# Optimization experiments

Hardware: AMD Instinct MI355X
Metric: run time of the kernel (lower is better)

## Reference

```python
import jax, jax.numpy as jnp
import numpy as np

H, W = 256, 336
FLOW_SCALING = float(max(H, W))  # max(config['loader']['resolution'])
REG_WEIGHT = 0.001               # config['loss']['flow_regul_weight']
B, N = 8, 262144


def setup_inputs() -> dict:
    key = jax.random.key(0)
    k1, k2, k3, k4, k5 = jax.random.split(key, 5)
    # small flow so a reasonable fraction of warped events stays in-bounds
    flow = 0.05 * jax.random.normal(k1, (B, 2, H, W), dtype=jnp.float32)
    ys = jax.random.randint(k2, (B, N), 0, H).astype(jnp.float32)
    xs = jax.random.randint(k3, (B, N), 0, W).astype(jnp.float32)
    ts = jax.random.uniform(k4, (B, N), dtype=jnp.float32)  # normalized timestamps in [0,1]
    pol = jax.random.randint(k5, (B, N), 0, 2)
    # event layout per the code: (ts, y, x, p)
    event_list = jnp.stack([ts, ys, xs, pol.astype(jnp.float32) * 2.0 - 1.0], axis=-1)
    pol_mask = jnp.stack([(pol == 1), (pol == 0)], axis=-1).astype(jnp.float32)  # [B,N,2]
    return {"flow": flow, "event_list": event_list, "pol_mask": pol_mask}


def _get_interpolation(events, event_flow, tref):
    # warped event coords (y, x): [B, N, 2]
    warped = events[:, :, 1:3] + (tref - events[:, :, 0:1]) * event_flow * FLOW_SCALING
    top_y = jnp.floor(warped[:, :, 0:1])
    bot_y = jnp.floor(warped[:, :, 0:1] + 1.0)
    left_x = jnp.floor(warped[:, :, 1:2])
    right_x = jnp.floor(warped[:, :, 1:2] + 1.0)
    # four bilinear corners stacked along event dim -> [B, 4N, 2]
    idx = jnp.concatenate([
        jnp.concatenate([top_y, left_x], -1),
        jnp.concatenate([top_y, right_x], -1),
        jnp.concatenate([bot_y, left_x], -1),
        jnp.concatenate([bot_y, right_x], -1)], axis=1)
    warped4 = jnp.tile(warped, (1, 4, 1))
    weights = jnp.maximum(0.0, 1.0 - jnp.abs(warped4 - idx))
    mask = ((idx[:, :, 0:1] >= 0) & (idx[:, :, 0:1] < H)
            & (idx[:, :, 1:2] >= 0) & (idx[:, :, 1:2] < W)).astype(weights.dtype)
    idx = idx * mask          # unfeasible indices -> 0
    weights = weights * mask  # unfeasible weights -> 0
    flat_idx = (idx[:, :, 0] * W + idx[:, :, 1]).astype(jnp.int32)  # [B, 4N]
    w = jnp.prod(weights, axis=-1, keepdims=True)                    # [B, 4N, 1]
    return flat_idx, w


def _interpolate(flat_idx, weights, polarity_mask):
    # scatter-add bilinear weights into an H*W image, per batch element
    w = (weights * polarity_mask)[:, :, 0]  # [B, 4N]
    return jax.vmap(lambda i, v: jax.ops.segment_sum(v, i, num_segments=H * W))(flat_idx, w)


def reference(flow, event_list, pol_mask):
    pol4 = jnp.tile(pol_mask, (1, 4, 1))              # [B, 4N, 2]
    ts4 = jnp.tile(event_list[:, :, 0:1], (1, 4, 1))  # [B, 4N, 1]
    # gather flow at original event pixel locations
    flow_idx = (event_list[:, :, 1] * W + event_list[:, :, 2]).astype(jnp.int32)  # [B, N]
    flow_flat = flow.reshape(flow.shape[0], 2, -1)
    event_flowy = jnp.take_along_axis(flow_flat[:, 1, :], flow_idx, axis=1)
    event_flowx = jnp.take_along_axis(flow_flat[:, 0, :], flow_idx, axis=1)
    event_flow = jnp.stack([event_flowy, event_flowx], axis=-1)  # [B, N, 2] (y, x)

    loss = jnp.float32(0.0)
    # forward warp (tref=1, avg ts) and backward warp (tref=0, avg 1-ts)
    for tref, tgrad in ((1.0, ts4), (0.0, 1.0 - ts4)):
        idx, wts = _get_interpolation(event_list, event_flow, tref)
        for p in range(2):  # positive / negative polarity
            pm = pol4[:, :, p:p + 1]
            iwe = _interpolate(idx, wts, pm)
            iwe_ts = _interpolate(idx, wts * tgrad, pm)
            loss = loss + jnp.sum((iwe_ts / (iwe + 1e-9)) ** 2)

    # charbonnier flow smoothness
    flow_dx = flow[:, :, :-1, :] - flow[:, :, 1:, :]
    flow_dy = flow[:, :, :, :-1] - flow[:, :, :, 1:]
    smooth = jnp.sum(jnp.sqrt(flow_dx ** 2 + 1e-6)) + jnp.sum(jnp.sqrt(flow_dy ** 2 + 1e-6))
    return loss + REG_WEIGHT * smooth
```

## Files before the change

### kernel.cpp

```cpp
#include <hip/hip_runtime.h>

#define HH 256
#define WW 336
#define HWPIX (HH * WW)
#define BATCH 8
#define NEV 262144
#define NEV_SHIFT 18
#define FLOW_SCALING 336.0f
#define REG_WEIGHT 0.001f

#define BANDS 32
#define BANDSHIFT 3
#define BANDROWS 8
#define NBINS (2 * BATCH * BANDS)
#define CAP 14336
#define GSTRIDE 16

#define BE_THREADS 1024
#define EVPT 2
#define EV_PER_BLOCK (BE_THREADS * EVPT)
#define MAXITEMS 8320

#define HTILE (BANDROWS * WW)
#define NBLK_ACC NBINS

#define GCOUNT_BYTES (NBINS * GSTRIDE * 4)
#define PK_BYTES ((size_t)NBINS * CAP * 4)
#define QY_BYTES ((size_t)NBINS * CAP * 2)

__device__ __forceinline__ float wave_reduce_sum(float v) {
    #pragma unroll
    for (int o = 32; o > 0; o >>= 1) v += __shfl_down(v, o, 64);
    return v;
}

__device__ __forceinline__ float charb(float d) { return sqrtf(d * d + 1e-6f); }

__global__ __launch_bounds__(256)
void flow_prep(const float* __restrict__ flow, float2* __restrict__ flowi,
               unsigned int* __restrict__ gcount, float* __restrict__ loss_acc,
               unsigned int* __restrict__ done_count,
               float* __restrict__ smooth_partial) {
    __shared__ float red[4];
    int tid = threadIdx.x;
    if (blockIdx.x == 0) {
        for (int i = tid; i < NBINS * GSTRIDE; i += 256) gcount[i] = 0u;
        if (tid == 0) { *loss_acc = 0.0f; *done_count = 0u; }
    }

    const int N4 = BATCH * HWPIX / 4;
    const int H4 = HWPIX / 4;
    const int W4 = WW / 4;
    float v = 0.0f;
    for (int i = blockIdx.x * 256 + tid; i < N4; i += gridDim.x * 256) {
        int b = i / H4, u = i - b * H4;
        int row = u / W4, c4 = u - row * W4;
        const float4* ch0 = (const float4*)(flow + (size_t)b * 2 * HWPIX);
        const float4* ch1 = ch0 + H4;
        float4 a0 = ch0[u];
        float4 a1 = ch1[u];

        float4* fo = (float4*)(flowi + (size_t)b * HWPIX);
        fo[2 * u]     = make_float4(a0.x, a1.x, a0.y, a1.y);
        fo[2 * u + 1] = make_float4(a0.z, a1.z, a0.w, a1.w);

        if (row < HH - 1) {
            float4 d0 = ch0[u + W4];
            float4 d1 = ch1[u + W4];
            v += charb(a0.x - d0.x) + charb(a0.y - d0.y) +
                 charb(a0.z - d0.z) + charb(a0.w - d0.w) +
                 charb(a1.x - d1.x) + charb(a1.y - d1.y) +
                 charb(a1.z - d1.z) + charb(a1.w - d1.w);
        }
        v += charb(a0.x - a0.y) + charb(a0.y - a0.z) + charb(a0.z - a0.w) +
             charb(a1.x - a1.y) + charb(a1.y - a1.z) + charb(a1.z - a1.w);
        if (c4 < W4 - 1) {
            float r0 = ((const float*)ch0)[4 * u + 4];
            float r1 = ((const float*)ch1)[4 * u + 4];
            v += charb(a0.w - r0) + charb(a1.w - r1);
        }
    }
    v = wave_reduce_sum(v);
    if ((tid & 63) == 0) red[tid >> 6] = v;
    __syncthreads();
    if (tid < 4) {
        float r = red[tid];
        r += __shfl_down(r, 2, 64);
        r += __shfl_down(r, 1, 64);
        if (tid == 0) smooth_partial[blockIdx.x] = r;
    }
}

__global__ __launch_bounds__(BE_THREADS)
void bin_events(const float2* __restrict__ flowi,
                const float4* __restrict__ ev,
                unsigned int* __restrict__ gcount,
                unsigned int* __restrict__ pk_arr,
                unsigned short* __restrict__ qy_arr) {
    __shared__ int lcnt[64];
    __shared__ int loff[64];
    __shared__ int gbase[64];
    __shared__ int stotal;
    __shared__ __align__(16) unsigned long long sval[MAXITEMS];

    int tid = threadIdx.x;
    if (tid < 64) lcnt[tid] = 0;
    __syncthreads();

    int base = blockIdx.x * EV_PER_BLOCK;
    int b = base >> NEV_SHIFT;
    const float2* fB = flowi + (size_t)b * HWPIX;

    unsigned int pkv[EVPT][2];
    unsigned int hiA[EVPT][2], hiB[EVPT][2];
    int rkA[EVPT][2], rkB[EVPT][2];

    #pragma unroll
    for (int e = 0; e < EVPT; ++e) {
        int bn = base + e * BE_THREADS + tid;
        float4 ee = ev[bn];
        float t = ee.x, y = ee.y, x = ee.z;
        unsigned int p = (ee.w > 0.0f) ? 0u : 1u;

        int iy = (int)y, ix = (int)x;
        float2 f = fB[iy * WW + ix];
        float fx = f.x, fy = f.y;

        #pragma unroll
        for (int tr = 0; tr < 2; ++tr) {
            rkA[e][tr] = -1; rkB[e][tr] = -1;
            float tref  = tr ? 0.0f : 1.0f;
            float tg    = tr ? (1.0f - t) : t;
            float dtS = (tref - t) * FLOW_SCALING;
            float wy = fmaf(dtS, fy, y);
            float wx = fmaf(dtS, fx, x);
            if (!(wx > -1.0f && wx < (float)WW)) continue;
            if (!(wy > -1.0f && wy < (float)HH)) continue;

            int ty = (int)floorf(wy);
            int band0 = -1, band1 = -1;
            if (ty >= 0 && ty < HH) band0 = ty >> BANDSHIFT;
            int r1 = ty + 1;
            if (r1 >= 0 && r1 < HH) {
                int bb = r1 >> BANDSHIFT;
                if (bb != band0) band1 = bb;
            }

            unsigned int qx = (unsigned int)(fmaf(wx, 2048.0f, 2048.5f));
            unsigned int qt = (unsigned int)(tg * 2047.0f + 0.5f);
            pkv[e][tr] = (qx << 12) | (qt << 1) | p;

            if (band0 >= 0) {
                float wyrel = wy - (float)(band0 * BANDROWS - 1);
                unsigned int qy = (unsigned int)fmaf(wyrel, 2048.0f, 0.5f);
                int lb = tr * BANDS + band0;
                hiA[e][tr] = qy | ((unsigned int)lb << 16);
                rkA[e][tr] = atomicAdd(&lcnt[lb], 1);
            }
            if (band1 >= 0) {
                float wyrel = wy - (float)(band1 * BANDROWS - 1);
                unsigned int qy = (unsigned int)fmaf(wyrel, 2048.0f, 0.5f);
                int lb = tr * BANDS + band1;
                hiB[e][tr] = qy | ((unsigned int)lb << 16);
                rkB[e][tr] = atomicAdd(&lcnt[lb], 1);
            }
        }
    }
    __syncthreads();

    if (tid < 64) {
        int c  = lcnt[tid];
        int ce = (c + 1) & ~1;
        int xg = ce;
        #pragma unroll
        for (int o = 1; o < 64; o <<= 1) {
            int yv = __shfl_up(xg, o, 64);
            if (tid >= o) xg += yv;
        }
        int lo = xg - ce;
        loff[tid] = lo;
        if (tid == 63) stotal = xg;
        int gbin = ((tid >> 5) * BATCH + b) * BANDS + (tid & 31);
        gbase[tid] = ce > 0 ? (int)atomicAdd(&gcount[gbin * GSTRIDE],
                                             (unsigned int)ce) : 0;
        if (c & 1) {
            unsigned int hi = (15u << 11) | ((unsigned int)tid << 16);
            sval[lo + c] = ((unsigned long long)hi << 32);
        }
    }
    __syncthreads();

    #pragma unroll
    for (int e = 0; e < EVPT; ++e) {
        #pragma unroll
        for (int tr = 0; tr < 2; ++tr) {
            if (rkA[e][tr] >= 0) {
                int lb = (hiA[e][tr] >> 16) & 63;
                sval[loff[lb] + rkA[e][tr]] =
                    (unsigned long long)pkv[e][tr] |
                    ((unsigned long long)hiA[e][tr] << 32);
            }
            if (rkB[e][tr] >= 0) {
                int lb = (hiB[e][tr] >> 16) & 63;
                sval[loff[lb] + rkB[e][tr]] =
                    (unsigned long long)pkv[e][tr] |
                    ((unsigned long long)hiB[e][tr] << 32);
            }
        }
    }
    __syncthreads();

    int total = stotal;
    for (int i = tid * 2; i < total; i += 2 * BE_THREADS) {
        uint4 two = *(const uint4*)&sval[i];
        unsigned int pk0 = two.x, h0 = two.y;
        unsigned int qy0 = h0 & 0xffffu;
        int lb0 = (h0 >> 16) & 63;
        int gs0 = gbase[lb0] + (i - loff[lb0]);
        int gbin0 = ((lb0 >> 5) * BATCH + b) * BANDS + (lb0 & 31);
        if (gs0 + 1 < CAP) {
            size_t s = (size_t)gbin0 * CAP + gs0;
            *(uint2*)(pk_arr + s) = make_uint2(pk0, two.z);
            *(unsigned int*)(qy_arr + s) = qy0 | ((two.w & 0xffffu) << 16);
        }
    }
}

__device__ __forceinline__ unsigned int pack_w(float w, float tg) {
    unsigned int lo16 = (unsigned int)fmaf(w, 1024.0f, 0.5f);
    unsigned int hi16 = (unsigned int)fmaf(w * tg, 1024.0f, 0.5f);
    return lo16 | (hi16 << 16);
}

__device__ __forceinline__ void accum_item(unsigned int* __restrict__ sA,
                                           unsigned int* __restrict__ sB,
                                           unsigned int pk, unsigned int qy) {
    unsigned int qx = pk >> 12;
    float tg = (float)((pk >> 1) & 2047u) * (1.0f / 2047.0f);
    int p = pk & 1u;

    int lx = (int)(qx >> 11) - 1;
    float fxx = (float)(qx & 2047u) * (1.0f / 2048.0f);

    int rowq = qy >> 11;
    float fy = (float)(qy & 2047u) * (1.0f / 2048.0f);
    int row_top = rowq - 1;

    unsigned int* A  = sA + p * HTILE;
    unsigned int* Bb = sB + p * HTILE;

    #pragma unroll
    for (int a = 0; a < 2; ++a) {
        int ry = row_top + a;
        if ((unsigned)ry >= (unsigned)BANDROWS) continue;
        float wrow = a ? fy : (1.0f - fy);
        int rb = ry * WW;
        if (lx >= 0 && lx + 1 < WW) {
            unsigned int pl = pack_w(wrow * (1.0f - fxx), tg);
            unsigned int pr = pack_w(wrow * fxx, tg);
            unsigned long long v =
                (unsigned long long)pl | ((unsigned long long)pr << 32);
            if (v == 0ull) continue;
            if ((lx & 1) == 0) {
                atomicAdd((unsigned long long*)(A + rb + lx), v);
            } else {
                atomicAdd((unsigned long long*)(Bb + rb + lx - 1), v);
            }
        } else if (lx == -1) {
            unsigned int pw = pack_w(wrow * fxx, tg);
            if (pw) atomicAdd(&A[rb], pw);
        } else if (lx == WW - 1) {
            unsigned int pw = pack_w(wrow * (1.0f - fxx), tg);
            if (pw) atomicAdd(&A[rb + lx], pw);
        }
    }
}

__global__ __launch_bounds__(1024)
void bin_accum(const unsigned int* __restrict__ gcount,
               const unsigned int* __restrict__ pk_arr,
               const unsigned short* __restrict__ qy_arr,
               const float* __restrict__ smooth_partial,
               float* __restrict__ loss_acc,
               unsigned int* __restrict__ done_count,
               float* __restrict__ out) {
    __shared__ __align__(16) unsigned int sA[2 * HTILE];
    __shared__ __align__(16) unsigned int sB[2 * HTILE];
    __shared__ float red[16];
    __shared__ int lastflag;

    int band = blockIdx.x;
    int tr   = blockIdx.y;
    int b    = blockIdx.z;
    int tid  = threadIdx.x;

    for (int i = tid; i < 2 * HTILE; i += 1024) { sA[i] = 0u; sB[i] = 0u; }
    __syncthreads();

    int gbin = (tr * BATCH + b) * BANDS + band;
    int cnt = min((int)gcount[gbin * GSTRIDE], CAP);
    const unsigned int* pkp = pk_arr + (size_t)gbin * CAP;
    const unsigned short* qyp = qy_arr + (size_t)gbin * CAP;
    const uint4* pk4 = (const uint4*)pkp;
    const uint4* qy8 = (const uint4*)qyp;

    int noct = cnt >> 3;
    if (tid < noct) {
        uint4 p0 = pk4[2 * tid], p1 = pk4[2 * tid + 1];
        uint4 q0 = qy8[tid];
        for (int n = tid + 1024; n < noct; n += 1024) {
            uint4 np0 = pk4[2 * n], np1 = pk4[2 * n + 1];
            uint4 nq0 = qy8[n];
            accum_item(sA, sB, p0.x, q0.x & 0xffffu);
            accum_item(sA, sB, p0.y, q0.x >> 16);
            accum_item(sA, sB, p0.z, q0.y & 0xffffu);
            accum_item(sA, sB, p0.w, q0.y >> 16);
            accum_item(sA, sB, p1.x, q0.z & 0xffffu);
            accum_item(sA, sB, p1.y, q0.z >> 16);
            accum_item(sA, sB, p1.z, q0.w & 0xffffu);
            accum_item(sA, sB, p1.w, q0.w >> 16);
            p0 = np0; p1 = np1; q0 = nq0;
        }
        accum_item(sA, sB, p0.x, q0.x & 0xffffu);
        accum_item(sA, sB, p0.y, q0.x >> 16);
        accum_item(sA, sB, p0.z, q0.y & 0xffffu);
        accum_item(sA, sB, p0.w, q0.y >> 16);
        accum_item(sA, sB, p1.x, q0.z & 0xffffu);
        accum_item(sA, sB, p1.y, q0.z >> 16);
        accum_item(sA, sB, p1.z, q0.w & 0xffffu);
        accum_item(sA, sB, p1.w, q0.w >> 16);
    }
    int done = noct << 3;
    int rem = cnt - done;
    if (tid < rem) {
        accum_item(sA, sB, pkp[done + tid], (unsigned int)qyp[done + tid]);
    }
    __syncthreads();

    float v = 0.0f;
    for (int i = tid; i < 2 * HTILE; i += 1024) {
        int px = i - (i / WW) * WW;
        unsigned int u = sA[i] + (px ? sB[i - 1] : 0u);
        float iwe = (float)(u & 0xffffu);
        float its = (float)(u >> 16);
        float r = its / (iwe + 1.024e-6f);
        v += r * r;
    }
    v = wave_reduce_sum(v);
    if ((tid & 63) == 0) red[tid >> 6] = v;
    __syncthreads();
    if (tid == 0) {
        float r = 0.0f;
        #pragma unroll
        for (int k = 0; k < 16; ++k) r += red[k];
        atomicAdd(loss_acc, r);
        __threadfence();
        unsigned int t = atomicAdd(done_count, 1u);
        lastflag = (t == (unsigned)(NBLK_ACC - 1));
    }
    __syncthreads();

    if (lastflag) {
        float pv = (tid < 512) ? smooth_partial[tid] : 0.0f;
        pv = wave_reduce_sum(pv);
        if ((tid & 63) == 0) red[tid >> 6] = pv;
        __syncthreads();
        if (tid == 0) {
            float sm = 0.0f;
            #pragma unroll
            for (int k = 0; k < 16; ++k) sm += red[k];
            float total = atomicAdd(loss_acc, 0.0f);
            *out = total + REG_WEIGHT * sm;
        }
    }
}

extern "C" void kernel_launch(void* const* d_in, const int* in_sizes, int n_in,
                              void* d_out, int out_size, void* d_ws, size_t ws_size,
                              hipStream_t stream) {
    const float*  flow  = (const float*)d_in[0];
    const float4* ev    = (const float4*)d_in[1];
    float* out = (float*)d_out;

    unsigned int*   gcount     = (unsigned int*)d_ws;
    float*          loss_acc   = (float*)((char*)d_ws + GCOUNT_BYTES);
    unsigned int*   done_count = (unsigned int*)((char*)d_ws + GCOUNT_BYTES + 4);
    float*          smooth_p   = (float*)((char*)d_ws + GCOUNT_BYTES + 512);
    unsigned int*   pk_arr     = (unsigned int*)((char*)d_ws + GCOUNT_BYTES + 4096);
    unsigned short* qy_arr     = (unsigned short*)((char*)d_ws + GCOUNT_BYTES + 4096 + PK_BYTES);
    float2*         flowi      = (float2*)((char*)d_ws + GCOUNT_BYTES + 4096 + PK_BYTES + QY_BYTES);

    flow_prep<<<512, 256, 0, stream>>>(flow, flowi, gcount, loss_acc,
                                       done_count, smooth_p);

    int total_ev = BATCH * NEV;
    bin_events<<<total_ev / EV_PER_BLOCK, BE_THREADS, 0, stream>>>(
        flowi, ev, gcount, pk_arr, qy_arr);

    dim3 g2(BANDS, 2, BATCH);
    bin_accum<<<g2, 1024, 0, stream>>>(gcount, pk_arr, qy_arr, smooth_p,
                                       loss_acc, done_count, out);
}
```

Before: 133.9 us.

## Move smoothness term into accumulation kernel and widen bin padding to four

The Charbonnier smoothness reduction moves out of flow_prep and into bin_accum, where each block handles a strided slice of the flow and folds the weighted sum into its loss contribution. This leaves flow_prep as a pure transpose and removes the separate partial-sum array and the final-block reduction. Bin counts are now padded to multiples of four instead of two, so the scatter from shared memory can write 16-byte pk and 8-byte qy stores, at the cost of more dummy padding items and a slightly larger shared buffer. The added flow reads in bin_accum may overlap with its atomic-heavy accumulation phase, but they also lengthen that kernel.

Result: no change. 133.3 us, median of 2 (-0.4%).

```diff
diff --git a/kernel.cpp b/kernel.cpp
--- a/kernel.cpp
+++ b/kernel.cpp
@@ -19,7 +19,7 @@
 #define BE_THREADS 1024
 #define EVPT 2
 #define EV_PER_BLOCK (BE_THREADS * EVPT)
-#define MAXITEMS 8320
+#define MAXITEMS 8384
 
 #define HTILE (BANDROWS * WW)
 #define NBLK_ACC NBINS
@@ -39,9 +39,7 @@
 __global__ __launch_bounds__(256)
 void flow_prep(const float* __restrict__ flow, float2* __restrict__ flowi,
                unsigned int* __restrict__ gcount, float* __restrict__ loss_acc,
-               unsigned int* __restrict__ done_count,
-               float* __restrict__ smooth_partial) {
-    __shared__ float red[4];
+               unsigned int* __restrict__ done_count) {
     int tid = threadIdx.x;
     if (blockIdx.x == 0) {
         for (int i = tid; i < NBINS * GSTRIDE; i += 256) gcount[i] = 0u;
@@ -50,11 +48,8 @@
 
     const int N4 = BATCH * HWPIX / 4;
     const int H4 = HWPIX / 4;
-    const int W4 = WW / 4;
-    float v = 0.0f;
     for (int i = blockIdx.x * 256 + tid; i < N4; i += gridDim.x * 256) {
         int b = i / H4, u = i - b * H4;
-        int row = u / W4, c4 = u - row * W4;
         const float4* ch0 = (const float4*)(flow + (size_t)b * 2 * HWPIX);
         const float4* ch1 = ch0 + H4;
         float4 a0 = ch0[u];
@@ -63,31 +58,6 @@
         float4* fo = (float4*)(flowi + (size_t)b * HWPIX);
         fo[2 * u]     = make_float4(a0.x, a1.x, a0.y, a1.y);
         fo[2 * u + 1] = make_float4(a0.z, a1.z, a0.w, a1.w);
-
-        if (row < HH - 1) {
-            float4 d0 = ch0[u + W4];
-            float4 d1 = ch1[u + W4];
-            v += charb(a0.x - d0.x) + charb(a0.y - d0.y) +
-                 charb(a0.z - d0.z) + charb(a0.w - d0.w) +
-                 charb(a1.x - d1.x) + charb(a1.y - d1.y) +
-                 charb(a1.z - d1.z) + charb(a1.w - d1.w);
-        }
-        v += charb(a0.x - a0.y) + charb(a0.y - a0.z) + charb(a0.z - a0.w) +
-             charb(a1.x - a1.y) + charb(a1.y - a1.z) + charb(a1.z - a1.w);
-        if (c4 < W4 - 1) {
-            float r0 = ((const float*)ch0)[4 * u + 4];
-            float r1 = ((const float*)ch1)[4 * u + 4];
-            v += charb(a0.w - r0) + charb(a1.w - r1);
-        }
-    }
-    v = wave_reduce_sum(v);
-    if ((tid & 63) == 0) red[tid >> 6] = v;
-    __syncthreads();
-    if (tid < 4) {
-        float r = red[tid];
-        r += __shfl_down(r, 2, 64);
-        r += __shfl_down(r, 1, 64);
-        if (tid == 0) smooth_partial[blockIdx.x] = r;
     }
 }
 
@@ -170,7 +140,7 @@
 
     if (tid < 64) {
         int c  = lcnt[tid];
-        int ce = (c + 1) & ~1;
+        int ce = (c + 3) & ~3;
         int xg = ce;
         #pragma unroll
         for (int o = 1; o < 64; o <<= 1) {
@@ -183,10 +153,9 @@
         int gbin = ((tid >> 5) * BATCH + b) * BANDS + (tid & 31);
         gbase[tid] = ce > 0 ? (int)atomicAdd(&gcount[gbin * GSTRIDE],
                                              (unsigned int)ce) : 0;
-        if (c & 1) {
-            unsigned int hi = (15u << 11) | ((unsigned int)tid << 16);
-            sval[lo + c] = ((unsigned long long)hi << 32);
-        }
+        unsigned int hi = (15u << 11) | ((unsigned int)tid << 16);
+        for (int j = c; j < ce; ++j)
+            sval[lo + j] = ((unsigned long long)hi << 32);
     }
     __syncthreads();
 
@@ -211,17 +180,18 @@
     __syncthreads();
 
     int total = stotal;
-    for (int i = tid * 2; i < total; i += 2 * BE_THREADS) {
-        uint4 two = *(const uint4*)&sval[i];
-        unsigned int pk0 = two.x, h0 = two.y;
-        unsigned int qy0 = h0 & 0xffffu;
-        int lb0 = (h0 >> 16) & 63;
+    for (int i = tid * 4; i < total; i += 4 * BE_THREADS) {
+        uint4 q0 = *(const uint4*)&sval[i];
+        uint4 q1 = *(const uint4*)&sval[i + 2];
+        int lb0 = (q0.y >> 16) & 63;
         int gs0 = gbase[lb0] + (i - loff[lb0]);
         int gbin0 = ((lb0 >> 5) * BATCH + b) * BANDS + (lb0 & 31);
-        if (gs0 + 1 < CAP) {
+        if (gs0 + 3 < CAP) {
             size_t s = (size_t)gbin0 * CAP + gs0;
-            *(uint2*)(pk_arr + s) = make_uint2(pk0, two.z);
-            *(unsigned int*)(qy_arr + s) = qy0 | ((two.w & 0xffffu) << 16);
+            *(uint4*)(pk_arr + s) = make_uint4(q0.x, q0.z, q1.x, q1.z);
+            *(uint2*)(qy_arr + s) = make_uint2(
+                (q0.y & 0xffffu) | ((q0.w & 0xffffu) << 16),
+                (q1.y & 0xffffu) | ((q1.w & 0xffffu) << 16));
         }
     }
 }
@@ -280,7 +250,7 @@
 void bin_accum(const unsigned int* __restrict__ gcount,
                const unsigned int* __restrict__ pk_arr,
                const unsigned short* __restrict__ qy_arr,
-               const float* __restrict__ smooth_partial,
+               const float* __restrict__ flow,
                float* __restrict__ loss_acc,
                unsigned int* __restrict__ done_count,
                float* __restrict__ out) {
@@ -293,6 +263,7 @@
     int tr   = blockIdx.y;
     int b    = blockIdx.z;
     int tid  = threadIdx.x;
+    int lblk = band + 32 * (tr + 2 * b);
 
     for (int i = tid; i < 2 * HTILE; i += 1024) { sA[i] = 0u; sB[i] = 0u; }
     __syncthreads();
@@ -335,6 +306,36 @@
     if (tid < rem) {
         accum_item(sA, sB, pkp[done + tid], (unsigned int)qyp[done + tid]);
     }
+
+    float sm = 0.0f;
+    {
+        const int N4 = BATCH * HWPIX / 4;
+        const int H4 = HWPIX / 4;
+        const int W4 = WW / 4;
+        for (int i = lblk * 1024 + tid; i < N4; i += NBLK_ACC * 1024) {
+            int bb = i / H4, u = i - bb * H4;
+            int row = u / W4, c4 = u - row * W4;
+            const float4* ch0 = (const float4*)(flow + (size_t)bb * 2 * HWPIX);
+            const float4* ch1 = ch0 + H4;
+            float4 a0 = ch0[u];
+            float4 a1 = ch1[u];
+            if (row < HH - 1) {
+                float4 d0 = ch0[u + W4];
+                float4 d1 = ch1[u + W4];
+                sm += charb(a0.x - d0.x) + charb(a0.y - d0.y) +
+                      charb(a0.z - d0.z) + charb(a0.w - d0.w) +
+                      charb(a1.x - d1.x) + charb(a1.y - d1.y) +
+                      charb(a1.z - d1.z) + charb(a1.w - d1.w);
+            }
+            sm += charb(a0.x - a0.y) + charb(a0.y - a0.z) + charb(a0.z - a0.w) +
+                  charb(a1.x - a1.y) + charb(a1.y - a1.z) + charb(a1.z - a1.w);
+            if (c4 < W4 - 1) {
+                float r0 = ((const float*)ch0)[4 * u + 4];
+                float r1 = ((const float*)ch1)[4 * u + 4];
+                sm += charb(a0.w - r0) + charb(a1.w - r1);
+            }
+        }
+    }
     __syncthreads();
 
     float v = 0.0f;
@@ -346,6 +347,7 @@
         float r = its / (iwe + 1.024e-6f);
         v += r * r;
     }
+    v = fmaf(sm, REG_WEIGHT, v);
     v = wave_reduce_sum(v);
     if ((tid & 63) == 0) red[tid >> 6] = v;
     __syncthreads();
@@ -360,18 +362,8 @@
     }
     __syncthreads();
 
-    if (lastflag) {
-        float pv = (tid < 512) ? smooth_partial[tid] : 0.0f;
-        pv = wave_reduce_sum(pv);
-        if ((tid & 63) == 0) red[tid >> 6] = pv;
-        __syncthreads();
-        if (tid == 0) {
-            float sm = 0.0f;
-            #pragma unroll
-            for (int k = 0; k < 16; ++k) sm += red[k];
-            float total = atomicAdd(loss_acc, 0.0f);
-            *out = total + REG_WEIGHT * sm;
-        }
+    if (lastflag && tid == 0) {
+        *out = atomicAdd(loss_acc, 0.0f);
     }
 }
 
@@ -385,19 +377,18 @@
     unsigned int*   gcount     = (unsigned int*)d_ws;
     float*          loss_acc   = (float*)((char*)d_ws + GCOUNT_BYTES);
     unsigned int*   done_count = (unsigned int*)((char*)d_ws + GCOUNT_BYTES + 4);
-    float*          smooth_p   = (float*)((char*)d_ws + GCOUNT_BYTES + 512);
     unsigned int*   pk_arr     = (unsigned int*)((char*)d_ws + GCOUNT_BYTES + 4096);
     unsigned short* qy_arr     = (unsigned short*)((char*)d_ws + GCOUNT_BYTES + 4096 + PK_BYTES);
     float2*         flowi      = (float2*)((char*)d_ws + GCOUNT_BYTES + 4096 + PK_BYTES + QY_BYTES);
 
     flow_prep<<<512, 256, 0, stream>>>(flow, flowi, gcount, loss_acc,
-                                       done_count, smooth_p);
+                                       done_count);
 
     int total_ev = BATCH * NEV;
     bin_events<<<total_ev / EV_PER_BLOCK, BE_THREADS, 0, stream>>>(
         flowi, ev, gcount, pk_arr, qy_arr);
 
     dim3 g2(BANDS, 2, BATCH);
-    bin_accum<<<g2, 1024, 0, stream>>>(gcount, pk_arr, qy_arr, smooth_p,
+    bin_accum<<<g2, 1024, 0, stream>>>(gcount, pk_arr, qy_arr, flow,
                                        loss_acc, done_count, out);
 }
```
